# Kernel tuning notes

Hardware: AMD Instinct MI355X
Metric: run time of the kernel (lower is better)

The kernel has to match this reference:

```python
import jax, jax.numpy as jnp
import numpy as np

EPS = 1e-5

def conv(x, w, groups=1):
    # x: NCHW, w: OIHW, VALID padding, stride 1 (cross-correlation, same as torch conv2d)
    return jax.lax.conv_general_dilated(x, w, (1, 1), 'VALID',
                                        feature_group_count=groups,
                                        dimension_numbers=('NCHW', 'OIHW', 'NCHW'))

def bn(x, g, b, m, v):
    # eval-mode batchnorm with running stats
    scale = (g / jnp.sqrt(v + EPS))[None, :, None, None]
    return (x - m[None, :, None, None]) * scale + b[None, :, None, None]

def xcorr_depthwise(x, k):
    # x: [B,C,Hs,Ws] search, k: [B,C,Hk,Wk] per-sample kernels
    B, C, H, W = x.shape
    xr = x.reshape(1, B * C, H, W)
    kr = k.reshape(B * C, 1, k.shape[2], k.shape[3])
    out = conv(xr, kr, groups=B * C)  # [1, B*C, Ho, Wo]
    return out.reshape(B, C, out.shape[2], out.shape[3])

def setup_inputs() -> dict:
    key = jax.random.key(0)
    ks = jax.random.split(key, 16)
    Cin, Hid, Cout = 256, 256, 20
    inp = {
        'kernel': jax.random.normal(ks[0], (128, Cin, 7, 7), jnp.float32),
        'search': jax.random.normal(ks[1], (128, Cin, 31, 31), jnp.float32),
        'wk': jax.random.normal(ks[2], (Hid, Cin, 3, 3), jnp.float32) * 0.02,
        'gk': jnp.ones((Hid,), jnp.float32),
        'bk': jnp.zeros((Hid,), jnp.float32),
        'mk': jax.random.normal(ks[3], (Hid,), jnp.float32) * 0.1,
        'vk': jax.random.uniform(ks[4], (Hid,), jnp.float32) + 0.5,
        'ws': jax.random.normal(ks[5], (Hid, Cin, 3, 3), jnp.float32) * 0.02,
        'gs': jnp.ones((Hid,), jnp.float32),
        'bs': jnp.zeros((Hid,), jnp.float32),
        'ms': jax.random.normal(ks[6], (Hid,), jnp.float32) * 0.1,
        'vs': jax.random.uniform(ks[7], (Hid,), jnp.float32) + 0.5,
        'wh1': jax.random.normal(ks[8], (Hid, Hid, 1, 1), jnp.float32) * 0.02,
        'gh': jnp.ones((Hid,), jnp.float32),
        'bh': jnp.zeros((Hid,), jnp.float32),
        'mh': jax.random.normal(ks[9], (Hid,), jnp.float32) * 0.1,
        'vh': jax.random.uniform(ks[10], (Hid,), jnp.float32) + 0.5,
        'wh2': jax.random.normal(ks[11], (Cout, Hid, 1, 1), jnp.float32) * 0.02,
        'bh2': jnp.zeros((Cout,), jnp.float32),
    }
    return inp

def reference(kernel, search, wk, gk, bk, mk, vk, ws, gs, bs, ms, vs,
              wh1, gh, bh, mh, vh, wh2, bh2):
    k = jax.nn.relu(bn(conv(kernel, wk), gk, bk, mk, vk))   # [B,256,5,5]
    s = jax.nn.relu(bn(conv(search, ws), gs, bs, ms, vs))   # [B,256,29,29]
    f = xcorr_depthwise(s, k)                               # [B,256,25,25]
    h = jax.nn.relu(bn(conv(f, wh1), gh, bh, mh, vh))
    out = conv(h, wh2) + bh2[None, :, None, None]           # [B,20,25,25]
    return out
```

## Files before the change

kernel.cpp:

```cpp
#include <hip/hip_runtime.h>

typedef __bf16 bf16x8 __attribute__((ext_vector_type(8)));
typedef float floatx4 __attribute__((ext_vector_type(4)));
typedef unsigned short u16;
typedef unsigned int u32;

__device__ __forceinline__ u16 f2bf(float f) {
    union { float f; unsigned int u; } q; q.f = f;
    unsigned int r = q.u + 0x7FFFu + ((q.u >> 16) & 1u);
    return (u16)(r >> 16);
}
__device__ __forceinline__ float bf2f(u16 b) {
    union { unsigned int u; float f; } q; q.u = ((unsigned int)b) << 16;
    return q.f;
}

__device__ __forceinline__ void gl2lds16(const u16* g, u16* l) {
    __builtin_amdgcn_global_load_lds((const __attribute__((address_space(1))) u32*)g,
                                     (__attribute__((address_space(3))) u32*)l, 16, 0, 0);
}


__global__ __launch_bounds__(256) void bn_prep(
    const float* __restrict__ gk, const float* __restrict__ bk,
    const float* __restrict__ mk, const float* __restrict__ vk,
    const float* __restrict__ gs, const float* __restrict__ bs,
    const float* __restrict__ ms, const float* __restrict__ vs,
    const float* __restrict__ gh, const float* __restrict__ bh,
    const float* __restrict__ mh, const float* __restrict__ vh,
    float* __restrict__ par)
{
    int i = threadIdx.x;
    float s;
    s = gk[i] * rsqrtf(vk[i] + 1e-5f); par[0*256+i] = s; par[1*256+i] = bk[i] - mk[i]*s;
    s = gs[i] * rsqrtf(vs[i] + 1e-5f); par[2*256+i] = s; par[3*256+i] = bs[i] - ms[i]*s;
    s = gh[i] * rsqrtf(vh[i] + 1e-5f); par[4*256+i] = s; par[5*256+i] = bh[i] - mh[i]*s;
}

__global__ __launch_bounds__(256) void pack3x3(const float* __restrict__ w, u16* __restrict__ out) {
    int tid = blockIdx.x * 256 + threadIdx.x;
    int o  = tid / 2304;
    int k  = tid - o * 2304;
    int rc = k >> 8;
    int ci = k & 255;
    out[tid] = f2bf(w[o * 2304 + ci * 9 + rc]);
}

__global__ __launch_bounds__(256) void cast_bf16(const float* __restrict__ in, u16* __restrict__ out, int n) {
    int tid = blockIdx.x * 256 + threadIdx.x;
    if (tid < n) out[tid] = f2bf(in[tid]);
}

__global__ __launch_bounds__(256) void nchw2nhwc_t(const float* __restrict__ in, u16* __restrict__ out,
                                                   int HW, int sptiles) {
    __shared__ float tile[64][33];
    int bid = blockIdx.x;
    int st  = bid % sptiles;
    int tmp = bid / sptiles;
    int ct  = tmp & 3;
    int b   = tmp >> 2;
    int sp0 = st * 32, ci0 = ct * 64;
    int t = threadIdx.x;
    int j = t & 31, i8 = t >> 5;
    const float* ip = in + ((size_t)b * 256 + ci0 + i8) * HW + sp0 + j;
#pragma unroll
    for (int k = 0; k < 8; ++k) {
        if (sp0 + j < HW) tile[i8 + k * 8][j] = ip[(size_t)(k * 8) * HW];
    }
    __syncthreads();
    int cl = t & 63, s4 = t >> 6;
#pragma unroll
    for (int k = 0; k < 8; ++k) {
        int spl = s4 + k * 4;
        int sp  = sp0 + spl;
        if (sp < HW) out[((size_t)b * HW + sp) * 256 + ci0 + cl] = f2bf(tile[cl][spl]);
    }
}

#define NS_BLK 421
__global__ __launch_bounds__(512, 2) void conv_gemm256(
    const u16* __restrict__ AinS, const u16* __restrict__ WpkS,
    const float* __restrict__ parS, u16* __restrict__ OutS,
    const u16* __restrict__ AinK, const u16* __restrict__ WpkK,
    const float* __restrict__ parK, u16* __restrict__ OutK)
{
    __shared__ __align__(16) u16 Alds[2][256][64];
    __shared__ __align__(16) u16 Blds[2][256][64];

    const int Ktot = 2304;
    const int NKT  = 36;
    const int KW   = 3;

    const int lid = blockIdx.x;
    const bool isk = (lid >= NS_BLK);

    int nid;
    if (!isk) {
        const int xcd = lid & 7, sub = lid >> 3;
        nid = (xcd < 5) ? (xcd * 53 + sub) : (265 + (xcd - 5) * 52 + sub);
    } else {
        nid = lid - NS_BLK;
    }
    const int m0 = nid << 8;

    const int OHW     = isk ? 25    : 841;
    const int OW      = isk ? 5     : 29;
    const int IW      = isk ? 7     : 31;
    const int bstride = isk ? 12544 : 246016;
    const int Mtot    = isk ? 3200  : 107648;
    const u16* Ain    = isk ? AinK : AinS;
    const u16* Wpk    = isk ? WpkK : WpkS;
    const float* scale = isk ? parK : parS;
    const float* shift = scale + 256;
    u16* Out          = isk ? OutK : OutS;

    const int t     = threadIdx.x;
    const int wave  = t >> 6;
    const int lane  = t & 63;
    const int lrow  = lane & 15;
    const int lquad = lane >> 4;
    const int wmBase = (wave >> 2) << 7;
    const int wnBase = (wave & 3) << 6;

    const u16* pA[4];
    const u16* pB[4];
#pragma unroll
    for (int j = 0; j < 4; ++j) {
        int u = j * 512 + t;
        int row = u >> 3, slot = u & 7;
        int ko = ((slot ^ (row & 7)) << 3);
        int m = m0 + row; if (m >= Mtot) m = Mtot - 1;
        int b = m / OHW; int rem = m - b * OHW; int y = rem / OW; int x = rem - y * OW;
        pA[j] = Ain + (size_t)b * bstride + (size_t)(y * IW + x) * 256 + ko;
        pB[j] = Wpk + (size_t)row * (size_t)Ktot + ko;
    }

    const int xo0 = ((lquad ^ (lrow & 7)) << 3);
    const int xo1 = xo0 ^ 32;

    floatx4 acc[8][4];
#pragma unroll
    for (int i = 0; i < 8; ++i)
#pragma unroll
        for (int j = 0; j < 4; ++j) acc[i][j] = (floatx4){0.f, 0.f, 0.f, 0.f};

#pragma unroll
    for (int j = 0; j < 4; ++j)
        gl2lds16(pA[j], &Alds[0][0][0] + j * 4096 + wave * 512);
#pragma unroll
    for (int j = 0; j < 4; ++j)
        gl2lds16(pB[j], &Blds[0][0][0] + j * 4096 + wave * 512);
    asm volatile("s_waitcnt vmcnt(0)" ::: "memory");
    __builtin_amdgcn_s_barrier();

#define LOADA(mb) do {                                              \
        const u16* _p = Ab + (wmBase + (mb) * 16 + lrow) * 64;      \
        aF[0][0] = *(const bf16x8*)(_p + xo0);                      \
        aF[0][1] = *(const bf16x8*)(_p + xo1);                      \
        aF[1][0] = *(const bf16x8*)(_p + 1024 + xo0);               \
        aF[1][1] = *(const bf16x8*)(_p + 1024 + xo1);               \
    } while (0)

#define MFMA16(mb) do {                                                                               \
        _Pragma("unroll")                                                                             \
        for (int _n = 0; _n < 4; ++_n) {                                                              \
            acc[(mb)][_n]     = __builtin_amdgcn_mfma_f32_16x16x32_bf16(aF[0][0], bB[_n][0], acc[(mb)][_n], 0, 0, 0);     \
            acc[(mb)][_n]     = __builtin_amdgcn_mfma_f32_16x16x32_bf16(aF[0][1], bB[_n][1], acc[(mb)][_n], 0, 0, 0);     \
            acc[(mb) + 1][_n] = __builtin_amdgcn_mfma_f32_16x16x32_bf16(aF[1][0], bB[_n][0], acc[(mb) + 1][_n], 0, 0, 0); \
            acc[(mb) + 1][_n] = __builtin_amdgcn_mfma_f32_16x16x32_bf16(aF[1][1], bB[_n][1], acc[(mb) + 1][_n], 0, 0, 0); \
        }                                                                                             \
    } while (0)

#define PH_MID() do {                                        \
        __builtin_amdgcn_s_barrier();                        \
        asm volatile("s_waitcnt lgkmcnt(0)" ::: "memory");   \
        __builtin_amdgcn_s_setprio(1);                       \
    } while (0)

#define PH_END() do {                                        \
        __builtin_amdgcn_s_setprio(0);                       \
        __builtin_amdgcn_s_barrier();                        \
    } while (0)

#pragma unroll 2
    for (int kt = 0; kt < NKT; ++kt) {
        const int c = kt & 1;
        const u16* Ab = &Alds[c][0][0];
        const u16* Bb = &Blds[c][0][0];
        u16* An = &Alds[c ^ 1][0][0];
        u16* Bn = &Blds[c ^ 1][0][0];
        const int pf = (kt + 1 < NKT);
        const int kt1 = kt + 1;
        const int rc = kt1 >> 2;
        const int rr = rc / KW;
        const int cc = rc - rr * KW;
        const int aoffA = (rr * IW + cc) * 256 + ((kt1 & 3) << 6);
        const int boffB = kt1 << 6;

        bf16x8 bB[4][2];
        bf16x8 aF[2][2];

#pragma unroll
        for (int ni = 0; ni < 4; ++ni) {
            const u16* _p = Bb + (wnBase + ni * 16 + lrow) * 64;
            bB[ni][0] = *(const bf16x8*)(_p + xo0);
            bB[ni][1] = *(const bf16x8*)(_p + xo1);
        }
        LOADA(0);
        if (pf) {
#pragma unroll
            for (int j = 0; j < 4; ++j)
                gl2lds16(pA[j] + aoffA, An + j * 4096 + wave * 512);
        }
        PH_MID();
        MFMA16(0);
        PH_END();

        LOADA(2);
        if (pf) {
#pragma unroll
            for (int j = 0; j < 4; ++j)
                gl2lds16(pB[j] + boffB, Bn + j * 4096 + wave * 512);
        }
        PH_MID();
        MFMA16(2);
        PH_END();

        LOADA(4);
        PH_MID();
        MFMA16(4);
        PH_END();

        LOADA(6);
        PH_MID();
        MFMA16(6);
        __builtin_amdgcn_s_setprio(0);
        asm volatile("s_waitcnt vmcnt(0)" ::: "memory");
        __builtin_amdgcn_s_barrier();
    }

#undef LOADA
#undef MFMA16
#undef PH_MID
#undef PH_END

    float sc[4], sh[4];
#pragma unroll
    for (int ni = 0; ni < 4; ++ni) {
        int gn = wnBase + ni * 16 + lrow;
        sc[ni] = scale[gn];
        sh[ni] = shift[gn];
    }
#pragma unroll
    for (int mi = 0; mi < 8; ++mi) {
        int gm0 = m0 + wmBase + mi * 16 + (lquad << 2);
#pragma unroll
        for (int ri = 0; ri < 4; ++ri) {
            int gm = gm0 + ri;
            if (gm < Mtot) {
                size_t ro = (size_t)gm * 256 + wnBase + lrow;
#pragma unroll
                for (int ni = 0; ni < 4; ++ni) {
                    float v = acc[mi][ni][ri] * sc[ni] + sh[ni];
                    v = fmaxf(v, 0.f);
                    Out[ro + ni * 16] = f2bf(v);
                }
            }
        }
    }
}

__global__ __launch_bounds__(256) void xcorr_head(
    const u16* __restrict__ ss, const u16* __restrict__ kk,
    const u16* __restrict__ w1, const float* __restrict__ parh,
    const float* __restrict__ w2, const float* __restrict__ b2,
    float* __restrict__ out)
{
    __shared__ __align__(16) u16   Flds[32 * 264];
    __shared__ __align__(16) float wl[20 * 260];

    int lid = blockIdx.x;
    int bid = (lid & 7) * 400 + (lid >> 3);
    int b = bid / 25, y = bid - b * 25;
    int t = threadIdx.x;

    for (int i = t; i < 1280; i += 256) {
        int co = i >> 6, c4 = i & 63;
        *(float4*)&wl[co * 260 + c4 * 4] = *(const float4*)&w2[(size_t)co * 256 + c4 * 4];
    }

    {
        int cg = (t & 31) << 3;
        int xg = t >> 5;
        const u16* kbase = kk + (size_t)b * 25 * 256 + cg;
        const u16* sbase = ss + (size_t)(b * 29 + y) * 29 * 256 + cg;

        float acc[4][8];
#pragma unroll
        for (int j = 0; j < 4; ++j)
#pragma unroll
            for (int e = 0; e < 8; ++e) acc[j][e] = 0.f;

#pragma unroll
        for (int r = 0; r < 5; ++r) {
            const u16* srow = sbase + (size_t)r * 29 * 256;
#pragma unroll
            for (int c = 0; c < 5; ++c) {
                bf16x8 kv = *(const bf16x8*)(kbase + (r * 5 + c) * 256);
                float kf[8];
#pragma unroll
                for (int e = 0; e < 8; ++e) kf[e] = (float)kv[e];
#pragma unroll
                for (int j = 0; j < 4; ++j) {
                    int x = xg + 8 * j;
                    if (x < 25) {
                        bf16x8 sv = *(const bf16x8*)(srow + (size_t)(x + c) * 256);
#pragma unroll
                        for (int e = 0; e < 8; ++e) acc[j][e] += (float)sv[e] * kf[e];
                    }
                }
            }
        }
#pragma unroll
        for (int j = 0; j < 4; ++j) {
            int x = xg + 8 * j;
            if (x < 25) {
                u16 pk[8];
#pragma unroll
                for (int e = 0; e < 8; ++e) pk[e] = f2bf(acc[j][e]);
                *(bf16x8*)&Flds[x * 264 + cg] = *(const bf16x8*)pk;
            }
        }
    }
    __syncthreads();

    {
        int wave = t >> 6, lane = t & 63;
        int lr = lane & 15, lq = lane >> 4;
        int nb = wave << 6;

        floatx4 hacc[2][4];
#pragma unroll
        for (int i = 0; i < 2; ++i)
#pragma unroll
            for (int j = 0; j < 4; ++j) hacc[i][j] = (floatx4){0.f, 0.f, 0.f, 0.f};

#pragma unroll
        for (int ks = 0; ks < 8; ++ks) {
            int ko = ks * 32 + lq * 8;
            bf16x8 a0 = *(const bf16x8*)&Flds[(lr)      * 264 + ko];
            bf16x8 a1 = *(const bf16x8*)&Flds[(16 + lr) * 264 + ko];
            bf16x8 bv[4];
#pragma unroll
            for (int ni = 0; ni < 4; ++ni)
                bv[ni] = *(const bf16x8*)&w1[(size_t)(nb + ni * 16 + lr) * 256 + ko];
#pragma unroll
            for (int ni = 0; ni < 4; ++ni) {
                hacc[0][ni] = __builtin_amdgcn_mfma_f32_16x16x32_bf16(a0, bv[ni], hacc[0][ni], 0, 0, 0);
                hacc[1][ni] = __builtin_amdgcn_mfma_f32_16x16x32_bf16(a1, bv[ni], hacc[1][ni], 0, 0, 0);
            }
        }

        float sc[4], sh[4];
#pragma unroll
        for (int ni = 0; ni < 4; ++ni) {
            int gn = nb + ni * 16 + lr;
            sc[ni] = parh[gn];
            sh[ni] = parh[256 + gn];
        }
        __syncthreads();
#pragma unroll
        for (int mt = 0; mt < 2; ++mt) {
#pragma unroll
            for (int reg = 0; reg < 4; ++reg) {
                int row = mt * 16 + lq * 4 + reg;
                if (row < 25) {
#pragma unroll
                    for (int ni = 0; ni < 4; ++ni) {
                        float v = hacc[mt][ni][reg] * sc[ni] + sh[ni];
                        v = fmaxf(v, 0.f);
                        Flds[row * 264 + nb + ni * 16 + lr] = f2bf(v);
                    }
                }
            }
        }
    }
    __syncthreads();

    for (int o = t; o < 500; o += 256) {
        int x = o / 20, co = o - x * 20;
        float acc = b2[co];
        const u16* hp = &Flds[x * 264];
        const float* wp = &wl[co * 260];
#pragma unroll 4
        for (int k = 0; k < 256; k += 8) {
            bf16x8 hv = *(const bf16x8*)(hp + k);
            float4 w0 = *(const float4*)(wp + k);
            float4 w1v = *(const float4*)(wp + k + 4);
            acc += (float)hv[0] * w0.x + (float)hv[1] * w0.y
                 + (float)hv[2] * w0.z + (float)hv[3] * w0.w
                 + (float)hv[4] * w1v.x + (float)hv[5] * w1v.y
                 + (float)hv[6] * w1v.z + (float)hv[7] * w1v.w;
        }
        out[(size_t)((b * 20 + co) * 25 + y) * 25 + x] = acc;
    }
}

#define OFF_SIN  0ull
#define SZ_SIN   62980096ull
#define OFF_KIN  (OFF_SIN + SZ_SIN)
#define SZ_KIN   3211264ull
#define OFF_WKP  (OFF_KIN + SZ_KIN)
#define SZ_WKP   1179648ull
#define OFF_WSP  (OFF_WKP + SZ_WKP)
#define SZ_WSP   1179648ull
#define OFF_WH1P (OFF_WSP + SZ_WSP)
#define SZ_WH1P  131072ull
#define OFF_PAR  (OFF_WH1P + SZ_WH1P)
#define SZ_PAR   8192ull
#define OFF_KK   (OFF_PAR + SZ_PAR)
#define SZ_KK    1638400ull
#define OFF_SS   (OFF_KK + SZ_KK)
#define SZ_SS    55115776ull

extern "C" void kernel_launch(void* const* d_in, const int* in_sizes, int n_in,
                              void* d_out, int out_size, void* d_ws, size_t ws_size,
                              hipStream_t stream) {
    const float* kin  = (const float*)d_in[0];
    const float* sin_ = (const float*)d_in[1];
    const float* wk   = (const float*)d_in[2];
    const float* gk   = (const float*)d_in[3];
    const float* bk   = (const float*)d_in[4];
    const float* mk   = (const float*)d_in[5];
    const float* vk   = (const float*)d_in[6];
    const float* wsw  = (const float*)d_in[7];
    const float* gs   = (const float*)d_in[8];
    const float* bs   = (const float*)d_in[9];
    const float* ms   = (const float*)d_in[10];
    const float* vs   = (const float*)d_in[11];
    const float* wh1  = (const float*)d_in[12];
    const float* gh   = (const float*)d_in[13];
    const float* bh   = (const float*)d_in[14];
    const float* mh   = (const float*)d_in[15];
    const float* vh   = (const float*)d_in[16];
    const float* wh2  = (const float*)d_in[17];
    const float* bh2  = (const float*)d_in[18];
    float* out = (float*)d_out;

    char* w = (char*)d_ws;
    u16*   SIN  = (u16*)(w + OFF_SIN);
    u16*   KIN  = (u16*)(w + OFF_KIN);
    u16*   WKP  = (u16*)(w + OFF_WKP);
    u16*   WSP  = (u16*)(w + OFF_WSP);
    u16*   WH1P = (u16*)(w + OFF_WH1P);
    float* PAR  = (float*)(w + OFF_PAR);
    u16*   KK   = (u16*)(w + OFF_KK);
    u16*   SS   = (u16*)(w + OFF_SS);

    bn_prep<<<1, 256, 0, stream>>>(gk, bk, mk, vk, gs, bs, ms, vs, gh, bh, mh, vh, PAR);
    pack3x3<<<2304, 256, 0, stream>>>(wk, WKP);
    pack3x3<<<2304, 256, 0, stream>>>(wsw, WSP);
    cast_bf16<<<256, 256, 0, stream>>>(wh1, WH1P, 65536);
    nchw2nhwc_t<<<128 * 4 * 2, 256, 0, stream>>>(kin, KIN, 49, 2);
    nchw2nhwc_t<<<128 * 4 * 31, 256, 0, stream>>>(sin_, SIN, 961, 31);

    conv_gemm256<<<434, 512, 0, stream>>>(SIN, WSP, PAR + 512, SS,
                                          KIN, WKP, PAR + 0, KK);
    xcorr_head<<<3200, 256, 0, stream>>>(SS, KK, WH1P, PAR + 1024, wh2, bh2, out);

    (void)in_sizes; (void)n_in; (void)out_size; (void)ws_size;
}
```

Baseline: 534.1 us.

## Merge prep kernels and split xcorr head into conv1 and head kernels

Combines the weight packing, BN parameter prep and the two layout transposes into two launches instead of six, cutting launch overhead. The fused xcorr/head kernel is split: the first kernel now writes the post-ReLU hidden activations to a global bf16 buffer (reusing the dead search-input region), and a new head kernel loads them with the 20x256 weights to compute the final 1x1 conv. This drops the LDS weight staging and a barrier from the heavy kernel, which may improve its occupancy, but adds a global round trip of about 40 MB and an extra launch.

```diff
diff --git a/kernel.cpp b/kernel.cpp
--- a/kernel.cpp
+++ b/kernel.cpp
@@ -20,41 +20,47 @@
                                      (__attribute__((address_space(3))) u32*)l, 16, 0, 0);
 }
 
-
-__global__ __launch_bounds__(256) void bn_prep(
+__global__ __launch_bounds__(256) void prep_all(
+    const float* __restrict__ wk, const float* __restrict__ wsw, const float* __restrict__ wh1,
     const float* __restrict__ gk, const float* __restrict__ bk,
     const float* __restrict__ mk, const float* __restrict__ vk,
     const float* __restrict__ gs, const float* __restrict__ bs,
     const float* __restrict__ ms, const float* __restrict__ vs,
     const float* __restrict__ gh, const float* __restrict__ bh,
     const float* __restrict__ mh, const float* __restrict__ vh,
+    u16* __restrict__ WKP, u16* __restrict__ WSP, u16* __restrict__ WH1P,
     float* __restrict__ par)
 {
-    int i = threadIdx.x;
-    float s;
-    s = gk[i] * rsqrtf(vk[i] + 1e-5f); par[0*256+i] = s; par[1*256+i] = bk[i] - mk[i]*s;
-    s = gs[i] * rsqrtf(vs[i] + 1e-5f); par[2*256+i] = s; par[3*256+i] = bs[i] - ms[i]*s;
-    s = gh[i] * rsqrtf(vh[i] + 1e-5f); par[4*256+i] = s; par[5*256+i] = bh[i] - mh[i]*s;
-}
-
-__global__ __launch_bounds__(256) void pack3x3(const float* __restrict__ w, u16* __restrict__ out) {
-    int tid = blockIdx.x * 256 + threadIdx.x;
-    int o  = tid / 2304;
-    int k  = tid - o * 2304;
-    int rc = k >> 8;
-    int ci = k & 255;
-    out[tid] = f2bf(w[o * 2304 + ci * 9 + rc]);
-}
-
-__global__ __launch_bounds__(256) void cast_bf16(const float* __restrict__ in, u16* __restrict__ out, int n) {
-    int tid = blockIdx.x * 256 + threadIdx.x;
-    if (tid < n) out[tid] = f2bf(in[tid]);
-}
-
-__global__ __launch_bounds__(256) void nchw2nhwc_t(const float* __restrict__ in, u16* __restrict__ out,
-                                                   int HW, int sptiles) {
+    int bid = blockIdx.x, t = threadIdx.x;
+    if (bid < 4608) {
+        const float* src = (bid < 2304) ? wk : wsw;
+        u16* dst = (bid < 2304) ? WKP : WSP;
+        int tid = ((bid < 2304) ? bid : bid - 2304) * 256 + t;
+        int o  = tid / 2304;
+        int k  = tid - o * 2304;
+        int rc = k >> 8;
+        int ci = k & 255;
+        dst[tid] = f2bf(src[o * 2304 + ci * 9 + rc]);
+    } else if (bid < 4864) {
+        int tid = (bid - 4608) * 256 + t;
+        WH1P[tid] = f2bf(wh1[tid]);
+    } else {
+        float s;
+        s = gk[t] * rsqrtf(vk[t] + 1e-5f); par[0*256+t] = s; par[1*256+t] = bk[t] - mk[t]*s;
+        s = gs[t] * rsqrtf(vs[t] + 1e-5f); par[2*256+t] = s; par[3*256+t] = bs[t] - ms[t]*s;
+        s = gh[t] * rsqrtf(vh[t] + 1e-5f); par[4*256+t] = s; par[5*256+t] = bh[t] - mh[t]*s;
+    }
+}
+
+__global__ __launch_bounds__(256) void nchw2nhwc_both(
+    const float* __restrict__ kin, u16* __restrict__ KIN,
+    const float* __restrict__ sin_, u16* __restrict__ SIN)
+{
     __shared__ float tile[64][33];
     int bid = blockIdx.x;
+    const float* in; u16* out; int HW, sptiles;
+    if (bid < 1024) { in = kin;  out = KIN; HW = 49;  sptiles = 2; }
+    else { bid -= 1024; in = sin_; out = SIN; HW = 961; sptiles = 31; }
     int st  = bid % sptiles;
     int tmp = bid / sptiles;
     int ct  = tmp & 3;
@@ -270,24 +276,17 @@
     }
 }
 
-__global__ __launch_bounds__(256) void xcorr_head(
+__global__ __launch_bounds__(256) void xcorr_conv1(
     const u16* __restrict__ ss, const u16* __restrict__ kk,
     const u16* __restrict__ w1, const float* __restrict__ parh,
-    const float* __restrict__ w2, const float* __restrict__ b2,
-    float* __restrict__ out)
+    u16* __restrict__ hh)
 {
-    __shared__ __align__(16) u16   Flds[32 * 264];
-    __shared__ __align__(16) float wl[20 * 260];
+    __shared__ __align__(16) u16 Flds[32 * 264];
 
     int lid = blockIdx.x;
     int bid = (lid & 7) * 400 + (lid >> 3);
     int b = bid / 25, y = bid - b * 25;
     int t = threadIdx.x;
-
-    for (int i = t; i < 1280; i += 256) {
-        int co = i >> 6, c4 = i & 63;
-        *(float4*)&wl[co * 260 + c4 * 4] = *(const float4*)&w2[(size_t)co * 256 + c4 * 4];
-    }
 
     {
         int cg = (t & 31) << 3;
@@ -368,7 +367,7 @@
             sc[ni] = parh[gn];
             sh[ni] = parh[256 + gn];
         }
-        __syncthreads();
+        u16* hrow = hh + (size_t)bid * 25 * 256;
 #pragma unroll
         for (int mt = 0; mt < 2; ++mt) {
 #pragma unroll
@@ -379,18 +378,35 @@
                     for (int ni = 0; ni < 4; ++ni) {
                         float v = hacc[mt][ni][reg] * sc[ni] + sh[ni];
                         v = fmaxf(v, 0.f);
-                        Flds[row * 264 + nb + ni * 16 + lr] = f2bf(v);
+                        hrow[row * 256 + nb + ni * 16 + lr] = f2bf(v);
                     }
                 }
             }
         }
     }
+}
+
+__global__ __launch_bounds__(256) void head(const u16* __restrict__ h, const float* __restrict__ w2,
+                                            const float* __restrict__ b2, float* __restrict__ out) {
+    __shared__ __align__(16) u16   hl[25 * 264];
+    __shared__ __align__(16) float wl[20 * 260];
+    int bid = blockIdx.x;
+    int b = bid / 25, y = bid - b * 25;
+    int t = threadIdx.x;
+    const u16* hrow = h + (size_t)(b * 25 + y) * 25 * 256;
+    for (int i = t; i < 800; i += 256) {
+        int x = i >> 5, c8 = i & 31;
+        *(bf16x8*)&hl[x * 264 + c8 * 8] = *(const bf16x8*)&hrow[i * 8];
+    }
+    for (int i = t; i < 1280; i += 256) {
+        int co = i >> 6, c4 = i & 63;
+        *(float4*)&wl[co * 260 + c4 * 4] = *(const float4*)&w2[(size_t)co * 256 + c4 * 4];
+    }
     __syncthreads();
-
     for (int o = t; o < 500; o += 256) {
         int x = o / 20, co = o - x * 20;
         float acc = b2[co];
-        const u16* hp = &Flds[x * 264];
+        const u16* hp = &hl[x * 264];
         const float* wp = &wl[co * 260];
 #pragma unroll 4
         for (int k = 0; k < 256; k += 8) {
@@ -422,6 +438,7 @@
 #define SZ_KK    1638400ull
 #define OFF_SS   (OFF_KK + SZ_KK)
 #define SZ_SS    55115776ull
+#define OFF_H    OFF_SIN
 
 extern "C" void kernel_launch(void* const* d_in, const int* in_sizes, int n_in,
                               void* d_out, int out_size, void* d_ws, size_t ws_size,
@@ -456,17 +473,17 @@
     float* PAR  = (float*)(w + OFF_PAR);
     u16*   KK   = (u16*)(w + OFF_KK);
     u16*   SS   = (u16*)(w + OFF_SS);
-
-    bn_prep<<<1, 256, 0, stream>>>(gk, bk, mk, vk, gs, bs, ms, vs, gh, bh, mh, vh, PAR);
-    pack3x3<<<2304, 256, 0, stream>>>(wk, WKP);
-    pack3x3<<<2304, 256, 0, stream>>>(wsw, WSP);
-    cast_bf16<<<256, 256, 0, stream>>>(wh1, WH1P, 65536);
-    nchw2nhwc_t<<<128 * 4 * 2, 256, 0, stream>>>(kin, KIN, 49, 2);
-    nchw2nhwc_t<<<128 * 4 * 31, 256, 0, stream>>>(sin_, SIN, 961, 31);
+    u16*   HH   = (u16*)(w + OFF_H);
+
+    prep_all<<<4865, 256, 0, stream>>>(wk, wsw, wh1,
+                                       gk, bk, mk, vk, gs, bs, ms, vs, gh, bh, mh, vh,
+                                       WKP, WSP, WH1P, PAR);
+    nchw2nhwc_both<<<1024 + 15872, 256, 0, stream>>>(kin, KIN, sin_, SIN);
 
     conv_gemm256<<<434, 512, 0, stream>>>(SIN, WSP, PAR + 512, SS,
                                           KIN, WKP, PAR + 0, KK);
-    xcorr_head<<<3200, 256, 0, stream>>>(SS, KK, WH1P, PAR + 1024, wh2, bh2, out);
+    xcorr_conv1<<<3200, 256, 0, stream>>>(SS, KK, WH1P, PAR + 1024, HH);
+    head<<<3200, 256, 0, stream>>>(HH, wh2, bh2, out);
 
     (void)in_sizes; (void)n_in; (void)out_size; (void)ws_size;
 }
```

Result: slower. 547.8 us (+2.6%).
